# Kernel tuning notes

Hardware: AMD Instinct MI355X
Metric: run time of the kernel (lower is better)

## Reference

```python
import jax, jax.numpy as jnp
import numpy as np
import math

N_HEADS = 16
EMBED = 1024
D_HEAD = EMBED // N_HEADS
B, L = 2, 2048


def setup_inputs() -> dict:
    key = jax.random.key(0)
    k1, k2, k3, k4, k5 = jax.random.split(key, 5)
    s = 0.02
    return {
        "x": jax.random.normal(k1, (B, L, EMBED), dtype=jnp.float32),
        "w_qkv": jax.random.normal(k2, (3 * EMBED, EMBED), dtype=jnp.float32) * s,
        "b_qkv": jax.random.normal(k3, (3 * EMBED,), dtype=jnp.float32) * s,
        "w_out": jax.random.normal(k4, (EMBED, EMBED), dtype=jnp.float32) * s,
        "b_out": jax.random.normal(k5, (EMBED,), dtype=jnp.float32) * s,
        "mask": 1,
    }


def reference(x, w_qkv, b_qkv, w_out, b_out, mask):
    b, l, e = x.shape
    qkv = x @ w_qkv.T + b_qkv                      # (B, L, 3E)
    q, k, v = jnp.split(qkv, 3, axis=-1)
    # (B, L, H, d) -> (B, H, L, d)
    q = q.reshape(b, l, N_HEADS, D_HEAD).transpose(0, 2, 1, 3)
    k = k.reshape(b, l, N_HEADS, D_HEAD).transpose(0, 2, 1, 3)
    v = v.reshape(b, l, N_HEADS, D_HEAD).transpose(0, 2, 1, 3)
    # NOTE: faithful to source bug -- scores use V, not K
    scores = jnp.einsum("bhld,bhmd->bhlm", q, v) * (1.0 / math.sqrt(D_HEAD))
    if mask:
        causal = jnp.triu(jnp.ones((l, l), dtype=bool), k=1)  # (L, L)
        scores = jnp.where(causal, -jnp.inf, scores)
    attn = jax.nn.softmax(scores, axis=-1)          # (B, H, L, L)
    out = jnp.einsum("bhlm,bhmd->bhld", attn, v)    # (B, H, L, d)
    # NOTE: faithful to source bug -- transpose(1,2) result discarded,
    # so reshape straight from (B, H, L, d) to (B, L, E)
    out = out.reshape(b, l, e)
    return out @ w_out.T + b_out
```

## Files before the change

### kernel.cpp

```cpp
#include <hip/hip_runtime.h>
#include <math.h>

constexpr int Lc = 2048, Ec = 1024, Hc = 16, Dc = 64;

typedef __attribute__((ext_vector_type(8))) short bf16x8;
typedef __attribute__((ext_vector_type(4))) float f32x4;
typedef unsigned short u16;
typedef unsigned int u32;

#define MFMA16(a, b, c) __builtin_amdgcn_mfma_f32_16x16x32_bf16(a, b, c, 0, 0, 0)

__device__ inline u16 f2bf(float f) {
  u32 u = __builtin_bit_cast(u32, f);
  u32 r = u + 0x7fff + ((u >> 16) & 1);
  return (u16)(r >> 16);
}

__device__ inline void gld16(const void* g, void* l) {
  __builtin_amdgcn_global_load_lds(
      (const __attribute__((address_space(1))) u32*)g,
      (__attribute__((address_space(3))) u32*)l, 16, 0, 0);
}

constexpr size_t XN = (size_t)4096 * 1024;
constexpr size_t WQN = (size_t)2048 * 1024;
constexpr size_t WON = (size_t)1024 * 1024;

__global__ __launch_bounds__(256) void convert_all(
    const float* __restrict__ x, const float* __restrict__ wqkv,
    const float* __restrict__ wout, u16* __restrict__ xb,
    u16* __restrict__ wqb, u16* __restrict__ wob)
{
  const size_t i = ((size_t)blockIdx.x * 256 + threadIdx.x) * 4;
  float4 v;
  u16* dst;
  if (i < XN) {
    v = *(const float4*)(x + i);
    dst = xb + i;
  } else if (i < XN + WQN) {
    const size_t off = i - XN;
    const size_t row = off >> 10, col = off & 1023;
    const size_t srow = row + ((row >> 10) << 10);
    v = *(const float4*)(wqkv + srow * 1024 + col);
    dst = wqb + off;
  } else {
    const size_t off = i - XN - WQN;
    v = *(const float4*)(wout + off);
    dst = wob + off;
  }
  u16 o0 = f2bf(v.x), o1 = f2bf(v.y), o2 = f2bf(v.z), o3 = f2bf(v.w);
  dst[0] = o0; dst[1] = o1; dst[2] = o2; dst[3] = o3;
}

__global__ __launch_bounds__(256) void gemm_qv(
    const u16* __restrict__ A, const u16* __restrict__ W,
    const float* __restrict__ bqkv, u16* __restrict__ Q, u16* __restrict__ V,
    u16* __restrict__ Vt)
{
  __shared__ __align__(16) u16 As[2][8192];
  __shared__ __align__(16) u16 Bs[2][8192];
  const int tid = threadIdx.x;
  const int w = tid >> 6, lane = tid & 63;
  const int quad = lane >> 4, l16 = lane & 15;
  const int wm = w >> 1, wn = w & 1;

  const int flat = blockIdx.x;
  const int xcd = flat & 7, s64 = flat >> 3;
  const int pr = xcd >> 1, pc = xcd & 1;
  const int rowTile = (pr * 8 + (s64 >> 3)) * 128;
  const int colTile = (pc * 8 + (s64 & 7)) * 128;

  const int srow = tid >> 3;
  const int e = (((tid & 7) * 16) ^ ((srow & 7) << 4)) >> 1;
  const u16* Asrc = A + (size_t)(rowTile + srow) * 1024 + e;
  const u16* Bsrc = W + (size_t)(colTile + srow) * 1024 + e;

  f32x4 acc[4][4] = {};

#define STAGE_QV(sb, k0)                                              \
  {                                                                   \
    gld16(Asrc + (k0),             &As[sb][tid * 8]);                 \
    gld16(Asrc + (k0) + 32 * 1024, &As[sb][tid * 8 + 2048]);          \
    gld16(Asrc + (k0) + 64 * 1024, &As[sb][tid * 8 + 4096]);          \
    gld16(Asrc + (k0) + 96 * 1024, &As[sb][tid * 8 + 6144]);          \
    gld16(Bsrc + (k0),             &Bs[sb][tid * 8]);                 \
    gld16(Bsrc + (k0) + 32 * 1024, &Bs[sb][tid * 8 + 2048]);          \
    gld16(Bsrc + (k0) + 64 * 1024, &Bs[sb][tid * 8 + 4096]);          \
    gld16(Bsrc + (k0) + 96 * 1024, &Bs[sb][tid * 8 + 6144]);          \
  }

  STAGE_QV(0, 0);
  int cur = 0;
  for (int k0 = 0; k0 < 1024; k0 += 64) {
    __syncthreads();
    if (k0 + 64 < 1024) STAGE_QV(cur ^ 1, k0 + 64);
    bf16x8 af[4][2], bf[4][2];
#pragma unroll
    for (int s = 0; s < 4; ++s)
#pragma unroll
      for (int kk = 0; kk < 2; ++kk)
        af[s][kk] = *(const bf16x8*)&As[cur][(wm * 64 + s * 16 + l16) * 64 +
                     ((kk * 32 + quad * 8) ^ ((l16 & 7) << 3))];
#pragma unroll
    for (int n = 0; n < 4; ++n)
#pragma unroll
      for (int kk = 0; kk < 2; ++kk)
        bf[n][kk] = *(const bf16x8*)&Bs[cur][(wn * 64 + n * 16 + l16) * 64 +
                     ((kk * 32 + quad * 8) ^ ((l16 & 7) << 3))];
#pragma unroll
    for (int kk = 0; kk < 2; ++kk)
#pragma unroll
      for (int s = 0; s < 4; ++s)
#pragma unroll
        for (int n = 0; n < 4; ++n)
          acc[s][n] = MFMA16(af[s][kk], bf[n][kk], acc[s][n]);
    cur ^= 1;
  }
#undef STAGE_QV

#pragma unroll
  for (int n = 0; n < 4; ++n) {
    const int gn = colTile + wn * 64 + n * 16 + l16;
    const bool isV = gn >= 1024;
    const float bias = bqkv[gn + (isV ? 1024 : 0)];
    const float scl = isV ? 1.0f : 0.125f;
    const int h = (gn & 1023) >> 6, d = gn & 63;
    u16* dst = isV ? V : Q;
#pragma unroll
    for (int s = 0; s < 4; ++s) {
      const int gm0 = rowTile + wm * 64 + s * 16 + quad * 4;
      const int b = gm0 >> 11;
      ushort4 tv;
#pragma unroll
      for (int r = 0; r < 4; ++r) {
        const int l = (gm0 + r) & 2047;
        const u16 val = f2bf((acc[s][n][r] + bias) * scl);
        dst[(((size_t)(b * Hc + h)) * Lc + l) * Dc + d] = val;
        ((u16*)&tv)[r] = val;
      }
      if (isV) {
        const int l0 = gm0 & 2047;
        *(ushort4*)(Vt + (((size_t)(b * Hc + h)) * Dc + d) * Lc + l0) = tv;
      }
    }
  }
}

constexpr int PSTR = 72;

__device__ inline void attn_half(
    const bf16x8 qf[2], const bf16x8 bv[4][2], const bf16x8 bvt[4][2],
    u16* __restrict__ Ps, f32x4 O[4], float lsum[4],
    int kt, int wq, bool needmask, int quad, int l16)
{
  f32x4 sf[4] = {};
#pragma unroll
  for (int nb = 0; nb < 4; ++nb) {
    sf[nb] = MFMA16(qf[0], bv[nb][0], sf[nb]);
    sf[nb] = MFMA16(qf[1], bv[nb][1], sf[nb]);
  }
#pragma unroll
  for (int nb = 0; nb < 4; ++nb)
#pragma unroll
    for (int r = 0; r < 4; ++r) {
      float p = __expf(sf[nb][r]);
      if (needmask) {
        const int key = kt + nb * 16 + l16;
        const int qr = wq + quad * 4 + r;
        if (key > qr) p = 0.f;
      }
      lsum[r] += p;
      Ps[(quad * 4 + r) * PSTR + nb * 16 + l16] = f2bf(p);
    }
  bf16x8 pf[2];
#pragma unroll
  for (int kk = 0; kk < 2; ++kk)
    pf[kk] = *(const bf16x8*)&Ps[l16 * PSTR + kk * 32 + quad * 8];
#pragma unroll
  for (int db = 0; db < 4; ++db) {
    O[db] = MFMA16(pf[0], bvt[db][0], O[db]);
    O[db] = MFMA16(pf[1], bvt[db][1], O[db]);
  }
}

__global__ __launch_bounds__(256) void attn_mfma(
    const u16* __restrict__ Q, const u16* __restrict__ V,
    const u16* __restrict__ Vt, u16* __restrict__ outA)
{
  __shared__ __align__(16) u16 lds[2 * 4096 + 2 * 4096 + 2 * 4 * 16 * PSTR];
  const int tid = threadIdx.x;
  const int w = tid >> 6, lane = tid & 63;
  const int quad = lane >> 4, l16 = lane & 15;

  const int flat = blockIdx.x;
  const int xcd = flat & 7, slot = flat >> 3;
  const int bh = xcd * 4 + (slot >> 4);
  const int xblk = slot & 15;
  const int b = bh >> 4, h = bh & 15;

  const u16* Qb = Q + (size_t)bh * Lc * Dc;
  const u16* Vb = V + (size_t)bh * Lc * Dc;
  const u16* Vtb = Vt + (size_t)bh * Dc * Lc;
  u16* Psl = &lds[16384 + w * 16 * PSTR];
  u16* Psh = &lds[16384 + (4 + w) * 16 * PSTR];

  const int b1 = tid * 16, b2 = b1 + 4096;
  const int e1 = (b1 ^ (((b1 >> 7) & 7) << 4)) >> 1;
  const int e2 = (b2 ^ (((b2 >> 7) & 7) << 4)) >> 1;
  const u16* vs1 = Vb + e1;
  const u16* vs2 = Vb + e2;
  const u16* ts1 = Vtb + (size_t)(e1 >> 6) * Lc + (e1 & 63);
  const u16* ts2 = Vtb + (size_t)(e2 >> 6) * Lc + (e2 & 63);

  int roff[4][2];
#pragma unroll
  for (int i = 0; i < 4; ++i)
#pragma unroll
    for (int kk = 0; kk < 2; ++kk) {
      const int byte = ((i * 16 + l16) << 7) + kk * 64 + quad * 16;
      roff[i][kk] = (byte ^ ((l16 & 7) << 4)) >> 1;
    }

  const int qlo = xblk, qhi = 31 - xblk;
  const int nt = qhi + 1;
  const int wqlo = qlo * 64 + w * 16;
  const int wqhi = qhi * 64 + w * 16;

  bf16x8 qfl[2], qfh[2];
#pragma unroll
  for (int kk = 0; kk < 2; ++kk) {
    qfl[kk] = *(const bf16x8*)(Qb + (size_t)(qlo * 64 + w * 16 + l16) * 64 + kk * 32 + quad * 8);
    qfh[kk] = *(const bf16x8*)(Qb + (size_t)(qhi * 64 + w * 16 + l16) * 64 + kk * 32 + quad * 8);
  }

  f32x4 Ol[4] = {}, Oh[4] = {};
  float lsl[4] = {0.f, 0.f, 0.f, 0.f}, lsh[4] = {0.f, 0.f, 0.f, 0.f};

  gld16(vs1, &lds[tid * 8]);
  gld16(vs2, &lds[2048 + tid * 8]);
  gld16(ts1, &lds[8192 + tid * 8]);
  gld16(ts2, &lds[8192 + 2048 + tid * 8]);

  int cur = 0;
  for (int t = 0; t < nt; ++t) {
    const int kt = t * 64;
    __syncthreads();
    if (t + 1 < nt) {
      const int sb = cur ^ 1, nk = kt + 64;
      gld16(vs1 + (size_t)nk * 64, &lds[sb * 4096 + tid * 8]);
      gld16(vs2 + (size_t)nk * 64, &lds[sb * 4096 + 2048 + tid * 8]);
      gld16(ts1 + nk, &lds[8192 + sb * 4096 + tid * 8]);
      gld16(ts2 + nk, &lds[8192 + sb * 4096 + 2048 + tid * 8]);
    }
    const u16* VsB = &lds[cur * 4096];
    const u16* VtB = &lds[8192 + cur * 4096];

    bf16x8 bv[4][2], bvt[4][2];
#pragma unroll
    for (int nb = 0; nb < 4; ++nb)
#pragma unroll
      for (int kk = 0; kk < 2; ++kk) {
        bv[nb][kk] = *(const bf16x8*)(VsB + roff[nb][kk]);
        bvt[nb][kk] = *(const bf16x8*)(VtB + roff[nb][kk]);
      }

    attn_half(qfh, bv, bvt, Psh, Oh, lsh, kt, wqhi, t == qhi, quad, l16);
    if (t <= qlo)
      attn_half(qfl, bv, bvt, Psl, Ol, lsl, kt, wqlo, t == qlo, quad, l16);
    cur ^= 1;
  }

#pragma unroll
  for (int half = 0; half < 2; ++half) {
    const int q0 = half ? qhi * 64 : qlo * 64;
    const f32x4* O = half ? Oh : Ol;
    const float* ls = half ? lsh : lsl;
#pragma unroll
    for (int r = 0; r < 4; ++r) {
      float l = ls[r];
      l += __shfl_xor(l, 1);
      l += __shfl_xor(l, 2);
      l += __shfl_xor(l, 4);
      l += __shfl_xor(l, 8);
      const float inv = 1.f / l;
      const int q = q0 + w * 16 + quad * 4 + r;
      const int orow = h * 128 + (q >> 4);
      const int cbase = (q & 15) << 6;
#pragma unroll
      for (int db = 0; db < 4; ++db)
        outA[((size_t)b * Lc + orow) * Ec + cbase + db * 16 + l16] =
            f2bf(O[db][r] * inv);
    }
  }
}

__global__ __launch_bounds__(256) void gemm_out(
    const u16* __restrict__ A, const u16* __restrict__ W,
    const float* __restrict__ bias, float* __restrict__ out)
{
  __shared__ __align__(16) u16 As[2][4096];
  __shared__ __align__(16) u16 Bs[2][8192];
  const int tid = threadIdx.x;
  const int w = tid >> 6, lane = tid & 63;
  const int quad = lane >> 4, l16 = lane & 15;
  const int wm = w >> 1, wn = w & 1;

  const int flat = blockIdx.x;
  const int xcd = flat & 7, s64 = flat >> 3;
  const int rowTile = (xcd * 8 + (s64 >> 3)) * 64;
  const int colTile = (s64 & 7) * 128;

  const int srow = tid >> 3;
  const int e = (((tid & 7) * 16) ^ ((srow & 7) << 4)) >> 1;
  const u16* Asrc = A + (size_t)(rowTile + srow) * 1024 + e;
  const u16* Bsrc = W + (size_t)(colTile + srow) * 1024 + e;

  f32x4 acc[2][4] = {};

#define STAGE_OUT(sb, k0)                                             \
  {                                                                   \
    gld16(Asrc + (k0),             &As[sb][tid * 8]);                 \
    gld16(Asrc + (k0) + 32 * 1024, &As[sb][tid * 8 + 2048]);          \
    gld16(Bsrc + (k0),             &Bs[sb][tid * 8]);                 \
    gld16(Bsrc + (k0) + 32 * 1024, &Bs[sb][tid * 8 + 2048]);          \
    gld16(Bsrc + (k0) + 64 * 1024, &Bs[sb][tid * 8 + 4096]);          \
    gld16(Bsrc + (k0) + 96 * 1024, &Bs[sb][tid * 8 + 6144]);          \
  }

  STAGE_OUT(0, 0);
  int cur = 0;
  for (int k0 = 0; k0 < 1024; k0 += 64) {
    __syncthreads();
    if (k0 + 64 < 1024) STAGE_OUT(cur ^ 1, k0 + 64);
    bf16x8 af[2][2], bf[4][2];
#pragma unroll
    for (int s = 0; s < 2; ++s)
#pragma unroll
      for (int kk = 0; kk < 2; ++kk)
        af[s][kk] = *(const bf16x8*)&As[cur][(wm * 32 + s * 16 + l16) * 64 +
                     ((kk * 32 + quad * 8) ^ ((l16 & 7) << 3))];
#pragma unroll
    for (int n = 0; n < 4; ++n)
#pragma unroll
      for (int kk = 0; kk < 2; ++kk)
        bf[n][kk] = *(const bf16x8*)&Bs[cur][(wn * 64 + n * 16 + l16) * 64 +
                     ((kk * 32 + quad * 8) ^ ((l16 & 7) << 3))];
#pragma unroll
    for (int kk = 0; kk < 2; ++kk)
#pragma unroll
      for (int s = 0; s < 2; ++s)
#pragma unroll
        for (int n = 0; n < 4; ++n)
          acc[s][n] = MFMA16(af[s][kk], bf[n][kk], acc[s][n]);
    cur ^= 1;
  }
#undef STAGE_OUT

#pragma unroll
  for (int n = 0; n < 4; ++n) {
    const int gn = colTile + wn * 64 + n * 16 + l16;
    const float bn = bias[gn];
#pragma unroll
    for (int s = 0; s < 2; ++s)
#pragma unroll
      for (int r = 0; r < 4; ++r) {
        const int gm = rowTile + wm * 32 + s * 16 + quad * 4 + r;
        out[(size_t)gm * 1024 + gn] = acc[s][n][r] + bn;
      }
  }
}

extern "C" void kernel_launch(void* const* d_in, const int* in_sizes, int n_in,
                              void* d_out, int out_size, void* d_ws, size_t ws_size,
                              hipStream_t stream) {
  (void)in_sizes; (void)n_in; (void)out_size; (void)ws_size;
  const float* x     = (const float*)d_in[0];
  const float* w_qkv = (const float*)d_in[1];
  const float* b_qkv = (const float*)d_in[2];
  const float* w_out = (const float*)d_in[3];
  const float* b_out = (const float*)d_in[4];
  float* out = (float*)d_out;

  u16* xb  = (u16*)d_ws;
  u16* wqb = xb + XN;
  u16* wob = wqb + WQN;
  u16* Qw  = wob + WON;
  u16* Vw  = Qw + (size_t)2 * Hc * Lc * Dc;
  u16* Vtw = Vw + (size_t)2 * Hc * Lc * Dc;
  u16* Aw  = Vtw + (size_t)2 * Hc * Lc * Dc;

  convert_all<<<7168, 256, 0, stream>>>(x, w_qkv, w_out, xb, wqb, wob);
  gemm_qv<<<512, 256, 0, stream>>>(xb, wqb, b_qkv, Qw, Vw, Vtw);
  attn_mfma<<<512, 256, 0, stream>>>(Qw, Vw, Vtw, Aw);
  gemm_out<<<512, 256, 0, stream>>>(Aw, wob, b_out, out);
}
```

Baseline: 171.6 us.

## Process four causal query tiles per attention block to reuse V tiles

Each attention block now handles four query tiles (p, 15-p, 16+p, 31-p) instead of two balanced ones, so every V/Vt tile loaded into LDS is shared by up to four query tiles, and the grid is halved to 256 blocks. The aim is to cut redundant global-to-LDS traffic and loop overhead while keeping causal work balanced across blocks. The P staging buffer is shrunk to one region per wave, which is reused across the sequential sub-tiles. The cost is more accumulator registers, fewer blocks for latency hiding on a device with 256 CUs, and possible serialization through the shared P buffer.

```diff
diff --git a/kernel.cpp b/kernel.cpp
--- a/kernel.cpp
+++ b/kernel.cpp
@@ -183,26 +183,47 @@
   }
 }
 
+__device__ inline void epi_half(
+    const f32x4 O[4], const float ls[4], int q0, int w, int quad, int l16,
+    int b, int h, u16* __restrict__ outA)
+{
+#pragma unroll
+  for (int r = 0; r < 4; ++r) {
+    float l = ls[r];
+    l += __shfl_xor(l, 1);
+    l += __shfl_xor(l, 2);
+    l += __shfl_xor(l, 4);
+    l += __shfl_xor(l, 8);
+    const float inv = 1.f / l;
+    const int q = q0 + w * 16 + quad * 4 + r;
+    const int orow = h * 128 + (q >> 4);
+    const int cbase = (q & 15) << 6;
+#pragma unroll
+    for (int db = 0; db < 4; ++db)
+      outA[((size_t)b * Lc + orow) * Ec + cbase + db * 16 + l16] =
+          f2bf(O[db][r] * inv);
+  }
+}
+
 __global__ __launch_bounds__(256) void attn_mfma(
     const u16* __restrict__ Q, const u16* __restrict__ V,
     const u16* __restrict__ Vt, u16* __restrict__ outA)
 {
-  __shared__ __align__(16) u16 lds[2 * 4096 + 2 * 4096 + 2 * 4 * 16 * PSTR];
+  __shared__ __align__(16) u16 lds[2 * 4096 + 2 * 4096 + 4 * 16 * PSTR];
   const int tid = threadIdx.x;
   const int w = tid >> 6, lane = tid & 63;
   const int quad = lane >> 4, l16 = lane & 15;
 
   const int flat = blockIdx.x;
   const int xcd = flat & 7, slot = flat >> 3;
-  const int bh = xcd * 4 + (slot >> 4);
-  const int xblk = slot & 15;
+  const int bh = xcd * 4 + (slot >> 3);
+  const int p = slot & 7;
   const int b = bh >> 4, h = bh & 15;
 
   const u16* Qb = Q + (size_t)bh * Lc * Dc;
   const u16* Vb = V + (size_t)bh * Lc * Dc;
   const u16* Vtb = Vt + (size_t)bh * Dc * Lc;
-  u16* Psl = &lds[16384 + w * 16 * PSTR];
-  u16* Psh = &lds[16384 + (4 + w) * 16 * PSTR];
+  u16* Ps = &lds[16384 + w * 16 * PSTR];
 
   const int b1 = tid * 16, b2 = b1 + 4096;
   const int e1 = (b1 ^ (((b1 >> 7) & 7) << 4)) >> 1;
@@ -221,20 +242,22 @@
       roff[i][kk] = (byte ^ ((l16 & 7) << 4)) >> 1;
     }
 
-  const int qlo = xblk, qhi = 31 - xblk;
-  const int nt = qhi + 1;
-  const int wqlo = qlo * 64 + w * 16;
-  const int wqhi = qhi * 64 + w * 16;
-
-  bf16x8 qfl[2], qfh[2];
+  const int q1 = p, q2 = 15 - p, q3 = 16 + p, q4 = 31 - p;
+  const int nt = q4 + 1;
+  const int wq1 = q1 * 64 + w * 16, wq2 = q2 * 64 + w * 16;
+  const int wq3 = q3 * 64 + w * 16, wq4 = q4 * 64 + w * 16;
+
+  bf16x8 qf1[2], qf2[2], qf3[2], qf4[2];
 #pragma unroll
   for (int kk = 0; kk < 2; ++kk) {
-    qfl[kk] = *(const bf16x8*)(Qb + (size_t)(qlo * 64 + w * 16 + l16) * 64 + kk * 32 + quad * 8);
-    qfh[kk] = *(const bf16x8*)(Qb + (size_t)(qhi * 64 + w * 16 + l16) * 64 + kk * 32 + quad * 8);
-  }
-
-  f32x4 Ol[4] = {}, Oh[4] = {};
-  float lsl[4] = {0.f, 0.f, 0.f, 0.f}, lsh[4] = {0.f, 0.f, 0.f, 0.f};
+    qf1[kk] = *(const bf16x8*)(Qb + (size_t)(wq1 + l16) * 64 + kk * 32 + quad * 8);
+    qf2[kk] = *(const bf16x8*)(Qb + (size_t)(wq2 + l16) * 64 + kk * 32 + quad * 8);
+    qf3[kk] = *(const bf16x8*)(Qb + (size_t)(wq3 + l16) * 64 + kk * 32 + quad * 8);
+    qf4[kk] = *(const bf16x8*)(Qb + (size_t)(wq4 + l16) * 64 + kk * 32 + quad * 8);
+  }
+
+  f32x4 O1[4] = {}, O2[4] = {}, O3[4] = {}, O4[4] = {};
+  float ls1[4] = {}, ls2[4] = {}, ls3[4] = {}, ls4[4] = {};
 
   gld16(vs1, &lds[tid * 8]);
   gld16(vs2, &lds[2048 + tid * 8]);
@@ -264,34 +287,17 @@
         bvt[nb][kk] = *(const bf16x8*)(VtB + roff[nb][kk]);
       }
 
-    attn_half(qfh, bv, bvt, Psh, Oh, lsh, kt, wqhi, t == qhi, quad, l16);
-    if (t <= qlo)
-      attn_half(qfl, bv, bvt, Psl, Ol, lsl, kt, wqlo, t == qlo, quad, l16);
+    attn_half(qf4, bv, bvt, Ps, O4, ls4, kt, wq4, t == q4, quad, l16);
+    if (t <= q3) attn_half(qf3, bv, bvt, Ps, O3, ls3, kt, wq3, t == q3, quad, l16);
+    if (t <= q2) attn_half(qf2, bv, bvt, Ps, O2, ls2, kt, wq2, t == q2, quad, l16);
+    if (t <= q1) attn_half(qf1, bv, bvt, Ps, O1, ls1, kt, wq1, t == q1, quad, l16);
     cur ^= 1;
   }
 
-#pragma unroll
-  for (int half = 0; half < 2; ++half) {
-    const int q0 = half ? qhi * 64 : qlo * 64;
-    const f32x4* O = half ? Oh : Ol;
-    const float* ls = half ? lsh : lsl;
-#pragma unroll
-    for (int r = 0; r < 4; ++r) {
-      float l = ls[r];
-      l += __shfl_xor(l, 1);
-      l += __shfl_xor(l, 2);
-      l += __shfl_xor(l, 4);
-      l += __shfl_xor(l, 8);
-      const float inv = 1.f / l;
-      const int q = q0 + w * 16 + quad * 4 + r;
-      const int orow = h * 128 + (q >> 4);
-      const int cbase = (q & 15) << 6;
-#pragma unroll
-      for (int db = 0; db < 4; ++db)
-        outA[((size_t)b * Lc + orow) * Ec + cbase + db * 16 + l16] =
-            f2bf(O[db][r] * inv);
-    }
-  }
+  epi_half(O1, ls1, q1 * 64, w, quad, l16, b, h, outA);
+  epi_half(O2, ls2, q2 * 64, w, quad, l16, b, h, outA);
+  epi_half(O3, ls3, q3 * 64, w, quad, l16, b, h, outA);
+  epi_half(O4, ls4, q4 * 64, w, quad, l16, b, h, outA);
 }
 
 __global__ __launch_bounds__(256) void gemm_out(
@@ -391,6 +397,6 @@
 
   convert_all<<<7168, 256, 0, stream>>>(x, w_qkv, w_out, xb, wqb, wob);
   gemm_qv<<<512, 256, 0, stream>>>(xb, wqb, b_qkv, Qw, Vw, Vtw);
-  attn_mfma<<<512, 256, 0, stream>>>(Qw, Vw, Vtw, Aw);
+  attn_mfma<<<256, 256, 0, stream>>>(Qw, Vw, Vtw, Aw);
   gemm_out<<<512, 256, 0, stream>>>(Aw, wob, b_out, out);
 }
```

Result: slower. 185.2 us (+7.9%).
